# Kernel tuning notes

Hardware: AMD Instinct MI355X
Metric: run time of the kernel (lower is better)

The kernel has to match this reference:

```python
import jax, jax.numpy as jnp
import numpy as np

B, S, N, C = 64, 512, 207, 1
H = 256
D = N * C          # flattened node-feature size (input_size * n_nodes)
DIN = 2 * D        # GRU input size with concat_mask=True


def setup_inputs() -> dict:
    key = jax.random.key(0)
    ks = jax.random.split(key, 8)
    x = jax.random.normal(ks[0], (B, S, N, C), dtype=jnp.float32)
    mask = (jax.random.uniform(ks[1], (B, S, N, C)) < 0.8).astype(jnp.float32)
    bnd = 1.0 / np.sqrt(H)  # torch default init bound for GRUCell and Linear(H, D)
    u = lambda k, shp: jax.random.uniform(k, shp, minval=-bnd, maxval=bnd, dtype=jnp.float32)
    return {
        'x': x,
        'mask': mask,
        'W_ih': u(ks[2], (3 * H, DIN)),
        'W_hh': u(ks[3], (3 * H, H)),
        'b_ih': u(ks[4], (3 * H,)),
        'b_hh': u(ks[5], (3 * H,)),
        'W_ro': u(ks[6], (D, H)),
        'b_ro': u(ks[7], (D,)),
    }


def _gru_cell(x_t, h, W_ih, W_hh, b_ih, b_hh):
    gi = x_t @ W_ih.T + b_ih              # [B, 3H]
    gh = h @ W_hh.T + b_hh                # [B, 3H]
    i_r, i_z, i_n = jnp.split(gi, 3, axis=-1)
    h_r, h_z, h_n = jnp.split(gh, 3, axis=-1)
    r = jax.nn.sigmoid(i_r + h_r)
    z = jax.nn.sigmoid(i_z + h_z)
    n = jnp.tanh(i_n + r * h_n)
    return (1.0 - z) * n + z * h


def reference(x, mask, W_ih, W_hh, b_ih, b_hh, W_ro, b_ro):
    b, s, n_nodes, c = x.shape
    xf = x.reshape(b, s, n_nodes * c)       # 'b s n c -> b s (n c)'
    mf = mask.reshape(b, s, n_nodes * c)
    h0 = jnp.zeros((b, H), dtype=x.dtype)   # state_init='zero'
    xhat0 = h0 @ W_ro.T + b_ro              # readout of initial state

    def step(carry, inp):
        h, x_hat = carry
        x_t, m_t = inp                       # [B, D] each
        x_p = jnp.where(m_t > 0.5, x_t, x_hat)
        x_in = jnp.concatenate([x_p, m_t], axis=-1)  # concat_mask
        h_new = _gru_cell(x_in, h, W_ih, W_hh, b_ih, b_hh)
        x_hat_new = h_new @ W_ro.T + b_ro
        return (h_new, x_hat_new), x_hat_new

    # scan over steps 0..S-2, time axis leading
    xs = (jnp.swapaxes(xf[:, :-1], 0, 1), jnp.swapaxes(mf[:, :-1], 0, 1))
    _, preds = jax.lax.scan(step, (h0, xhat0), xs)           # [S-1, B, D]
    preds = jnp.concatenate([xhat0[None], preds], axis=0)    # [S, B, D]
    x_hat = jnp.swapaxes(preds, 0, 1).reshape(b, s, n_nodes, c)
    return x_hat
```

## Files before the change

kernel.cpp:

```cpp
#include <hip/hip_runtime.h>
#include <math.h>

#define BB 64
#define SS 512
#define DD 207
#define HH 256
#define NWG 64
#define LDW 676
#define ROW 260
#define AG __HIP_MEMORY_SCOPE_AGENT

#define SROWS 672
#define HOFF  416
#define SLOT  (SROWS * 64)
#define BUF_FLOATS ((size_t)SS * SLOT)
#define FLAG_U32 (64 * 32)
#define STAGE_FLOATS ((size_t)SS * DD * 64)
#define WS_NEED6 ((BUF_FLOATS + FLAG_U32 + STAGE_FLOATS) * sizeof(float))

#define V3_AROWS 928
#define V3_HBASE 416
#define V3_ACT (V3_AROWS * 64)
#define V3_FLAGS (64 * 32)
#define V3_WS_SMALL ((size_t)(V3_ACT + V3_FLAGS) * sizeof(float))
#define V3_WS_FULL  ((size_t)(V3_ACT + V3_FLAGS + STAGE_FLOATS) * sizeof(float))

__device__ __forceinline__ void ast4(float* p, float v) {
    union { float f; unsigned u; } c; c.f = v;
    __hip_atomic_store((unsigned*)p, c.u, __ATOMIC_RELAXED, AG);
}

__device__ __forceinline__ void run_range6(
    const float4* __restrict__ A4, const float* __restrict__ wgl,
    float* __restrict__ red, int u, int bp, int wc0, int gr0, int len, int slot)
{
    float4 c0 = make_float4(0.f, 0.f, 0.f, 0.f);
    float4 c1 = c0, c2 = c0;
    #pragma unroll 4
    for (int k = 0; k < len; k += 4) {
        float4 a0 = A4[(gr0 + k + 0) * 16 + bp];
        float4 a1 = A4[(gr0 + k + 1) * 16 + bp];
        float4 a2 = A4[(gr0 + k + 2) * 16 + bp];
        float4 a3 = A4[(gr0 + k + 3) * 16 + bp];
        float4 w0 = *(const float4*)&wgl[(0 + u) * LDW + wc0 + k];
        float4 w1 = *(const float4*)&wgl[(4 + u) * LDW + wc0 + k];
        float4 w2 = *(const float4*)&wgl[(8 + u) * LDW + wc0 + k];
        c0.x += a0.x*w0.x + a1.x*w0.y + a2.x*w0.z + a3.x*w0.w;
        c0.y += a0.y*w0.x + a1.y*w0.y + a2.y*w0.z + a3.y*w0.w;
        c0.z += a0.z*w0.x + a1.z*w0.y + a2.z*w0.z + a3.z*w0.w;
        c0.w += a0.w*w0.x + a1.w*w0.y + a2.w*w0.z + a3.w*w0.w;
        c1.x += a0.x*w1.x + a1.x*w1.y + a2.x*w1.z + a3.x*w1.w;
        c1.y += a0.y*w1.x + a1.y*w1.y + a2.y*w1.z + a3.y*w1.w;
        c1.z += a0.z*w1.x + a1.z*w1.y + a2.z*w1.z + a3.z*w1.w;
        c1.w += a0.w*w1.x + a1.w*w1.y + a2.w*w1.z + a3.w*w1.w;
        c2.x += a0.x*w2.x + a1.x*w2.y + a2.x*w2.z + a3.x*w2.w;
        c2.y += a0.y*w2.x + a1.y*w2.y + a2.y*w2.z + a3.y*w2.w;
        c2.z += a0.z*w2.x + a1.z*w2.y + a2.z*w2.z + a3.z*w2.w;
        c2.w += a0.w*w2.x + a1.w*w2.y + a2.w*w2.z + a3.w*w2.w;
    }
    float4* R4 = (float4*)red;
    R4[(slot * 12 + 0 + u) * 16 + bp] = c0;
    R4[(slot * 12 + 4 + u) * 16 + bp] = c1;
    R4[(slot * 12 + 8 + u) * 16 + bp] = c2;
}

__global__ __launch_bounds__(256) void rnn_init6(float* __restrict__ ws) {
    int i = blockIdx.x * blockDim.x + threadIdx.x;
    for (int idx = i; idx < HH * 64; idx += gridDim.x * blockDim.x)
        ws[HOFF * 64 + idx] = 0.f;
    unsigned* fl = (unsigned*)(ws + BUF_FLOATS);
    for (int idx = i; idx < FLAG_U32; idx += gridDim.x * blockDim.x)
        fl[idx] = 0u;
}

__global__ __launch_bounds__(256) void rnn_persist6(
    const float* __restrict__ x, const float* __restrict__ mask,
    const float* __restrict__ W_ih, const float* __restrict__ W_hh,
    const float* __restrict__ b_ih, const float* __restrict__ b_hh,
    const float* __restrict__ W_ro, const float* __restrict__ b_ro,
    float* __restrict__ ws, float* __restrict__ out)
{
    const int wg = blockIdx.x;
    const int tid = threadIdx.x;
    const int lane = tid & 63;
    const int wv = tid >> 6;

    float* buf = ws;
    unsigned* flags = (unsigned*)(ws + BUF_FLOATS);
    float* stage = ws + BUF_FLOATS + FLAG_U32;

    __shared__ float wgl[12 * LDW];
    __shared__ float wrol[4 * ROW];
    __shared__ float red[8 * 12 * 64];
    __shared__ float redB[16 * 64];
    __shared__ float hloc[4 * 64];
    __shared__ float bihl[12], bhhl[12], brol[4];

    const int d0 = (207 * wg) / NWG;
    const int d1 = (207 * (wg + 1)) / NWG;
    const int dc = d1 - d0;

    for (int i = tid; i < 12 * LDW; i += 256) {
        int r = i / LDW, c = i - r * LDW;
        int rg = (r >> 2) * 256 + wg * 4 + (r & 3);
        float v = 0.f;
        if (c < 414) v = W_ih[rg * 414 + c];
        else if (c >= 416 && c < 672) v = W_hh[rg * 256 + (c - 416)];
        wgl[i] = v;
    }
    for (int i = tid; i < 4 * 256; i += 256) {
        int dl_ = i >> 8, j = i & 255;
        wrol[dl_ * ROW + j] = (dl_ < dc) ? W_ro[(d0 + dl_) * 256 + j] : 0.f;
    }
    if (tid < 12) {
        int rg = (tid >> 2) * 256 + wg * 4 + (tid & 3);
        bihl[tid] = b_ih[rg];
        bhhl[tid] = b_hh[rg];
    }
    if (tid < 4) brol[tid] = (tid < dc) ? b_ro[d0 + tid] : 0.f;
    hloc[tid] = 0.f;
    __syncthreads();

    const float4* A4 = (const float4*)buf;
    const int u  = lane >> 4;
    const int bp = lane & 15;

    const bool have = (tid < dc * 64);
    const int dl = tid >> 6, b = tid & 63;
    const size_t gbase = (size_t)b * (SS * DD) + (d0 + dl);
    float xv_pf = 0.f, mv_pf = 0.f;
    if (have) { xv_pf = x[gbase]; mv_pf = mask[gbase]; }

    unsigned gen = 0;

    for (int t = 0; t < SS; ++t) {
        const int sbase = t * SROWS;

        {
            const float* hrow = buf + (size_t)(sbase + HOFF) * 64;
            const int jb = wv * 64;
            float acc0 = 0.f, acc1 = 0.f, acc2 = 0.f, acc3 = 0.f;
            #pragma unroll 4
            for (int j = 0; j < 64; j += 4) {
                float a0 = hrow[(jb + j + 0) * 64 + lane];
                float a1 = hrow[(jb + j + 1) * 64 + lane];
                float a2 = hrow[(jb + j + 2) * 64 + lane];
                float a3 = hrow[(jb + j + 3) * 64 + lane];
                float4 w0 = *(const float4*)&wrol[0 * ROW + jb + j];
                float4 w1 = *(const float4*)&wrol[1 * ROW + jb + j];
                float4 w2 = *(const float4*)&wrol[2 * ROW + jb + j];
                float4 w3 = *(const float4*)&wrol[3 * ROW + jb + j];
                acc0 += a0*w0.x + a1*w0.y + a2*w0.z + a3*w0.w;
                acc1 += a0*w1.x + a1*w1.y + a2*w1.z + a3*w1.w;
                acc2 += a0*w2.x + a1*w2.y + a2*w2.z + a3*w2.w;
                acc3 += a0*w3.x + a1*w3.y + a2*w3.z + a3*w3.w;
            }
            redB[(wv * 4 + 0) * 64 + lane] = acc0;
            redB[(wv * 4 + 1) * 64 + lane] = acc1;
            redB[(wv * 4 + 2) * 64 + lane] = acc2;
            redB[(wv * 4 + 3) * 64 + lane] = acc3;
        }
        __syncthreads();
        if (have) {
            float xh = redB[(0 * 4 + dl) * 64 + b] + redB[(1 * 4 + dl) * 64 + b]
                     + redB[(2 * 4 + dl) * 64 + b] + redB[(3 * 4 + dl) * 64 + b]
                     + brol[dl];
            stage[(t * DD + d0 + dl) * 64 + b] = xh;
            if (t < SS - 1) {
                float xi = (mv_pf > 0.5f) ? xv_pf : xh;
                ast4(&buf[(size_t)(sbase + d0 + dl) * 64 + b], xi);
                ast4(&buf[(size_t)(sbase + 207 + d0 + dl) * 64 + b], mv_pf);
            }
        }
        if (t == SS - 1) break;

        ++gen;
        asm volatile("s_waitcnt vmcnt(0)" ::: "memory");
        __syncthreads();
        if (tid == 0)
            __hip_atomic_store(&flags[wg * 32], gen, __ATOMIC_RELAXED, AG);

        run_range6(A4, wgl, red, u, bp, 416 + wv * 64, sbase + HOFF + wv * 64, 64, 4 + wv);

        if (tid < 64) {
            unsigned* f = &flags[tid * 32];
            while (__hip_atomic_load(f, __ATOMIC_RELAXED, AG) < gen) {}
        }
        __syncthreads();

        run_range6(A4, wgl, red, u, bp, wv * 104, sbase + wv * 104, 104, wv);
        __syncthreads();

        {
            const int u2 = tid >> 6, b2 = tid & 63;
            float gir = bihl[0 + u2], giz = bihl[4 + u2], gin = bihl[8 + u2];
            float ghr = bhhl[0 + u2], ghz = bhhl[4 + u2], ghn = bhhl[8 + u2];
            #pragma unroll
            for (int s = 0; s < 4; ++s) {
                gir += red[(s * 12 + 0 + u2) * 64 + b2];
                giz += red[(s * 12 + 4 + u2) * 64 + b2];
                gin += red[(s * 12 + 8 + u2) * 64 + b2];
                ghr += red[((4 + s) * 12 + 0 + u2) * 64 + b2];
                ghz += red[((4 + s) * 12 + 4 + u2) * 64 + b2];
                ghn += red[((4 + s) * 12 + 8 + u2) * 64 + b2];
            }
            float r = 1.f / (1.f + __expf(-(gir + ghr)));
            float z = 1.f / (1.f + __expf(-(giz + ghz)));
            float n = tanhf(gin + r * ghn);
            float hn = (1.f - z) * n + z * hloc[u2 * 64 + b2];
            hloc[u2 * 64 + b2] = hn;
            ast4(&buf[(size_t)((t + 1) * SROWS + HOFF + wg * 4 + u2) * 64 + b2], hn);
        }

        ++gen;
        asm volatile("s_waitcnt vmcnt(0)" ::: "memory");
        __syncthreads();
        if (tid == 0)
            __hip_atomic_store(&flags[wg * 32], gen, __ATOMIC_RELAXED, AG);

        if (have && t + 1 < SS - 1) {
            xv_pf = x[gbase + (size_t)(t + 1) * DD];
            mv_pf = mask[gbase + (size_t)(t + 1) * DD];
        }

        if (tid < 64) {
            unsigned* f = &flags[tid * 32];
            while (__hip_atomic_load(f, __ATOMIC_RELAXED, AG) < gen) {}
        }
        __syncthreads();
    }
}

__global__ __launch_bounds__(256) void out_transpose(
    const float* __restrict__ stage, float* __restrict__ out)
{
    __shared__ float lds[DD * 65];
    const int t = blockIdx.x;
    const float* st = stage + (size_t)t * DD * 64;
    for (int i = threadIdx.x; i < DD * 64; i += 256) {
        int d = i >> 6, b = i & 63;
        lds[d * 65 + b] = st[i];
    }
    __syncthreads();
    for (int i = threadIdx.x; i < DD * 64; i += 256) {
        int b = i / DD, d = i - b * DD;
        out[(size_t)b * (SS * DD) + (size_t)t * DD + d] = lds[d * 65 + b];
    }
}

__device__ __forceinline__ void v3_gbar(unsigned* flags, int wg, unsigned g) {
    __syncthreads();
    if (threadIdx.x < 64) {
        if (threadIdx.x == 0) {
            __builtin_amdgcn_fence(__ATOMIC_RELEASE, "agent");
            __hip_atomic_store(&flags[wg * 32], g, __ATOMIC_RELAXED, AG);
        }
        unsigned* f = &flags[threadIdx.x * 32];
        while (__hip_atomic_load(f, __ATOMIC_RELAXED, AG) < g) { }
        __builtin_amdgcn_fence(__ATOMIC_ACQUIRE, "agent");
    }
    __syncthreads();
}

__global__ __launch_bounds__(256) void v3_init(float* __restrict__ ws) {
    int i = blockIdx.x * blockDim.x + threadIdx.x;
    const int nz = (672 - 414) * 64;
    for (int idx = i; idx < nz; idx += gridDim.x * blockDim.x)
        ws[414 * 64 + idx] = 0.f;
    for (int idx = i; idx < V3_FLAGS; idx += gridDim.x * blockDim.x)
        ((unsigned*)(ws + V3_ACT))[idx] = 0u;
}

template<bool STAGE>
__global__ __launch_bounds__(256) void v3_persist(
    const float* __restrict__ x, const float* __restrict__ mask,
    const float* __restrict__ W_ih, const float* __restrict__ W_hh,
    const float* __restrict__ b_ih, const float* __restrict__ b_hh,
    const float* __restrict__ W_ro, const float* __restrict__ b_ro,
    float* __restrict__ ws, float* __restrict__ out)
{
    const int wg = blockIdx.x;
    const int tid = threadIdx.x;
    const int lane = tid & 63;
    const int wv = tid >> 6;

    float* actg = ws;
    unsigned* flags = (unsigned*)(ws + V3_ACT);
    float* stage = ws + V3_ACT + V3_FLAGS;

    __shared__ float wgl[12 * LDW];
    __shared__ float wrol[4 * 256];
    __shared__ float red[5 * 12 * 64];
    __shared__ float redB[16 * 64];
    __shared__ float hloc[4 * 64];
    __shared__ float bihl[12], bhhl[12], brol[4];

    const int d0 = (207 * wg) / NWG;
    const int d1 = (207 * (wg + 1)) / NWG;
    const int dc = d1 - d0;

    for (int i = tid; i < 12 * LDW; i += 256) {
        int r = i / LDW, c = i - r * LDW;
        int rg = (r >> 2) * 256 + wg * 4 + (r & 3);
        float v = 0.f;
        if (c < 414) v = W_ih[rg * 414 + c];
        else if (c >= 416 && c < 672) v = W_hh[rg * 256 + (c - 416)];
        wgl[i] = v;
    }
    for (int i = tid; i < 4 * 256; i += 256) {
        int dl_ = i >> 8, j = i & 255;
        wrol[i] = (dl_ < dc) ? W_ro[(d0 + dl_) * 256 + j] : 0.f;
    }
    if (tid < 12) {
        int rg = (tid >> 2) * 256 + wg * 4 + (tid & 3);
        bihl[tid] = b_ih[rg];
        bhhl[tid] = b_hh[rg];
    }
    if (tid < 4) brol[tid] = (tid < dc) ? b_ro[d0 + tid] : 0.f;
    hloc[tid] = 0.f;
    __syncthreads();

    const float4* A4 = (const float4*)actg;
    const int u = lane >> 4;
    const int bp = lane & 15;

    const bool have = (tid < dc * 64);
    const int dl = tid >> 6, b = tid & 63;
    const size_t gbase = (size_t)b * (SS * DD) + (d0 + dl);
    float xv_pf = 0.f, mv_pf = 0.f;
    if (have) { xv_pf = x[gbase]; mv_pf = mask[gbase]; }

    unsigned gen = 0;

    for (int t = 0; t < SS; ++t) {
        const int par = t & 1;
        const int hrow0 = V3_HBASE + par * 256;

        {
            const float* hrow = actg + hrow0 * 64;
            const int jb = wv * 64;
            float acc0 = 0.f, acc1 = 0.f, acc2 = 0.f, acc3 = 0.f;
            #pragma unroll 4
            for (int j = 0; j < 64; j += 4) {
                float a0 = hrow[(jb + j + 0) * 64 + lane];
                float a1 = hrow[(jb + j + 1) * 64 + lane];
                float a2 = hrow[(jb + j + 2) * 64 + lane];
                float a3 = hrow[(jb + j + 3) * 64 + lane];
                float4 w0 = *(const float4*)&wrol[0 * 256 + jb + j];
                float4 w1 = *(const float4*)&wrol[1 * 256 + jb + j];
                float4 w2 = *(const float4*)&wrol[2 * 256 + jb + j];
                float4 w3 = *(const float4*)&wrol[3 * 256 + jb + j];
                acc0 += a0*w0.x + a1*w0.y + a2*w0.z + a3*w0.w;
                acc1 += a0*w1.x + a1*w1.y + a2*w1.z + a3*w1.w;
                acc2 += a0*w2.x + a1*w2.y + a2*w2.z + a3*w2.w;
                acc3 += a0*w3.x + a1*w3.y + a2*w3.z + a3*w3.w;
            }
            redB[(wv * 4 + 0) * 64 + lane] = acc0;
            redB[(wv * 4 + 1) * 64 + lane] = acc1;
            redB[(wv * 4 + 2) * 64 + lane] = acc2;
            redB[(wv * 4 + 3) * 64 + lane] = acc3;
        }
        __syncthreads();
        if (have) {
            float xh = redB[(0 * 4 + dl) * 64 + b] + redB[(1 * 4 + dl) * 64 + b]
                     + redB[(2 * 4 + dl) * 64 + b] + redB[(3 * 4 + dl) * 64 + b]
                     + brol[dl];
            if (STAGE) stage[(t * DD + d0 + dl) * 64 + b] = xh;
            else       out[gbase + (size_t)t * DD] = xh;
            if (t < SS - 1) {
                float xi = (mv_pf > 0.5f) ? xv_pf : xh;
                actg[(d0 + dl) * 64 + b] = xi;
                actg[(207 + d0 + dl) * 64 + b] = mv_pf;
            }
        }
        if (t == SS - 1) break;

        if (have && t + 1 < SS - 1) {
            xv_pf = x[gbase + (size_t)(t + 1) * DD];
            mv_pf = mask[gbase + (size_t)(t + 1) * DD];
        }

        v3_gbar(flags, wg, ++gen);

        if (wv == 0)      run_range6(A4, wgl, red, u, bp, 0,   0,          168, 0);
        else if (wv == 1) run_range6(A4, wgl, red, u, bp, 168, 168,        168, 1);
        else if (wv == 2) {
            run_range6(A4, wgl, red, u, bp, 336, 336,        80,  2);
            run_range6(A4, wgl, red, u, bp, 416, hrow0,      96,  3);
        } else            run_range6(A4, wgl, red, u, bp, 512, hrow0 + 96, 160, 4);
        __syncthreads();
        {
            const int u2 = tid >> 6, b2 = tid & 63;
            float gir = red[(0*12 + 0 + u2)*64 + b2] + red[(1*12 + 0 + u2)*64 + b2]
                      + red[(2*12 + 0 + u2)*64 + b2] + bihl[0 + u2];
            float giz = red[(0*12 + 4 + u2)*64 + b2] + red[(1*12 + 4 + u2)*64 + b2]
                      + red[(2*12 + 4 + u2)*64 + b2] + bihl[4 + u2];
            float gin = red[(0*12 + 8 + u2)*64 + b2] + red[(1*12 + 8 + u2)*64 + b2]
                      + red[(2*12 + 8 + u2)*64 + b2] + bihl[8 + u2];
            float ghr = red[(3*12 + 0 + u2)*64 + b2] + red[(4*12 + 0 + u2)*64 + b2] + bhhl[0 + u2];
            float ghz = red[(3*12 + 4 + u2)*64 + b2] + red[(4*12 + 4 + u2)*64 + b2] + bhhl[4 + u2];
            float ghn = red[(3*12 + 8 + u2)*64 + b2] + red[(4*12 + 8 + u2)*64 + b2] + bhhl[8 + u2];
            float r = 1.f / (1.f + __expf(-(gir + ghr)));
            float z = 1.f / (1.f + __expf(-(giz + ghz)));
            float n = tanhf(gin + r * ghn);
            float hn = (1.f - z) * n + z * hloc[u2 * 64 + b2];
            hloc[u2 * 64 + b2] = hn;
            actg[(V3_HBASE + (par ^ 1) * 256 + wg * 4 + u2) * 64 + b2] = hn;
        }
        v3_gbar(flags, wg, ++gen);
    }
}

__global__ __launch_bounds__(768) void rnn_fallback(
    const float* __restrict__ x, const float* __restrict__ mask,
    const float* __restrict__ W_ih, const float* __restrict__ W_hh,
    const float* __restrict__ b_ih, const float* __restrict__ b_hh,
    const float* __restrict__ W_ro, const float* __restrict__ b_ro,
    float* __restrict__ out)
{
    const int b = blockIdx.x, tid = threadIdx.x;
    __shared__ float h[HH];
    __shared__ float hnew[HH];
    __shared__ float xin[414 + 2];
    __shared__ float gi[768];
    __shared__ float gh[768];
    __shared__ float xhat[DD];
    const float bih = b_ih[tid], bhh = b_hh[tid];
    const float bro = (tid < DD) ? b_ro[tid] : 0.f;
    if (tid < HH) h[tid] = 0.f;
    if (tid < DD) xhat[tid] = bro;
    __syncthreads();
    const float* xb = x + (size_t)b * SS * DD;
    const float* mb = mask + (size_t)b * SS * DD;
    float* ob = out + (size_t)b * SS * DD;
    for (int t = 0; t < SS; ++t) {
        if (tid < DD) ob[t * DD + tid] = xhat[tid];
        if (t == SS - 1) break;
        if (tid < DD) {
            float m = mb[t * DD + tid], xv = xb[t * DD + tid];
            xin[tid] = (m > 0.5f) ? xv : xhat[tid];
            xin[DD + tid] = m;
        }
        __syncthreads();
        float accI = bih, accH = bhh;
        const float* wi = W_ih + (size_t)tid * 414;
        for (int k = 0; k < 414; ++k) accI += wi[k] * xin[k];
        const float* wh = W_hh + (size_t)tid * HH;
        for (int k = 0; k < HH; ++k) accH += wh[k] * h[k];
        gi[tid] = accI; gh[tid] = accH;
        __syncthreads();
        if (tid < HH) {
            float r = 1.f / (1.f + __expf(-(gi[tid] + gh[tid])));
            float z = 1.f / (1.f + __expf(-(gi[HH + tid] + gh[HH + tid])));
            float n = tanhf(gi[2 * HH + tid] + r * gh[2 * HH + tid]);
            hnew[tid] = (1.f - z) * n + z * h[tid];
        }
        __syncthreads();
        if (tid < DD) {
            float acc = bro;
            const float* wr = W_ro + (size_t)tid * HH;
            for (int k = 0; k < HH; ++k) acc += wr[k] * hnew[k];
            xhat[tid] = acc;
        }
        if (tid < HH) h[tid] = hnew[tid];
        __syncthreads();
    }
}

extern "C" void kernel_launch(void* const* d_in, const int* in_sizes, int n_in,
                              void* d_out, int out_size, void* d_ws, size_t ws_size,
                              hipStream_t stream) {
    const float* x    = (const float*)d_in[0];
    const float* mask = (const float*)d_in[1];
    const float* W_ih = (const float*)d_in[2];
    const float* W_hh = (const float*)d_in[3];
    const float* b_ih = (const float*)d_in[4];
    const float* b_hh = (const float*)d_in[5];
    const float* W_ro = (const float*)d_in[6];
    const float* b_ro = (const float*)d_in[7];
    float* out = (float*)d_out;
    float* ws  = (float*)d_ws;

    if (ws_size >= WS_NEED6) {
        hipLaunchKernelGGL(rnn_init6, dim3(64), dim3(256), 0, stream, ws);
        hipLaunchKernelGGL(rnn_persist6, dim3(NWG), dim3(256), 0, stream,
                           x, mask, W_ih, W_hh, b_ih, b_hh, W_ro, b_ro, ws, out);
        hipLaunchKernelGGL(out_transpose, dim3(SS), dim3(256), 0, stream,
                           ws + BUF_FLOATS + FLAG_U32, out);
    } else if (ws_size >= V3_WS_FULL) {
        hipLaunchKernelGGL(v3_init, dim3(32), dim3(256), 0, stream, ws);
        hipLaunchKernelGGL((v3_persist<true>), dim3(NWG), dim3(256), 0, stream,
                           x, mask, W_ih, W_hh, b_ih, b_hh, W_ro, b_ro, ws, out);
        hipLaunchKernelGGL(out_transpose, dim3(SS), dim3(256), 0, stream,
                           ws + V3_ACT + V3_FLAGS, out);
    } else if (ws_size >= V3_WS_SMALL) {
        hipLaunchKernelGGL(v3_init, dim3(32), dim3(256), 0, stream, ws);
        hipLaunchKernelGGL((v3_persist<false>), dim3(NWG), dim3(256), 0, stream,
                           x, mask, W_ih, W_hh, b_ih, b_hh, W_ro, b_ro, ws, out);
    } else {
        hipLaunchKernelGGL(rnn_fallback, dim3(BB), dim3(768), 0, stream,
                           x, mask, W_ih, W_hh, b_ih, b_hh, W_ro, b_ro, out);
    }
}
```

Baseline: 6.140 ms.

## Pin persistent GRU workgroups to a single XCD with 512-thread blocks

Launches 256 workgroups, reads each one's XCC id from a hardware register, and keeps only 32 blocks that land on the same XCD. Each surviving 512-thread block owns 8 hidden units instead of 4, which halves the number of participants in the per-step global barrier. When a probe confirms that all ranks share one XCD and see each other's writes, activation and hidden-state stores become plain stores instead of agent-scope atomics. The goal is to shorten the cross-workgroup barrier and make shared state cheaper to exchange through a single XCD's L2, at the cost of a more complex election handshake. It also leaves most of the device idle and depends on at least 32 blocks being scheduled on one XCD.

```diff
diff --git a/kernel.cpp b/kernel.cpp
--- a/kernel.cpp
+++ b/kernel.cpp
@@ -5,7 +5,6 @@
 #define SS 512
 #define DD 207
 #define HH 256
-#define NWG 64
 #define LDW 676
 #define ROW 260
 #define AG __HIP_MEMORY_SCOPE_AGENT
@@ -16,7 +15,14 @@
 #define BUF_FLOATS ((size_t)SS * SLOT)
 #define FLAG_U32 (64 * 32)
 #define STAGE_FLOATS ((size_t)SS * DD * 64)
-#define WS_NEED6 ((BUF_FLOATS + FLAG_U32 + STAGE_FLOATS) * sizeof(float))
+#define WS_NEED7 ((BUF_FLOATS + FLAG_U32 + STAGE_FLOATS) * sizeof(float))
+#define NW 32
+#define BS7 512
+#define GRID7 256
+#define HWREG_XCC (20 | (31 << 11))
+#define MAGICF 1.0e30f
+
+#define R0 ((size_t)(SS - 1) * SLOT)
 
 #define V3_AROWS 928
 #define V3_HBASE 416
@@ -24,10 +30,323 @@
 #define V3_FLAGS (64 * 32)
 #define V3_WS_SMALL ((size_t)(V3_ACT + V3_FLAGS) * sizeof(float))
 #define V3_WS_FULL  ((size_t)(V3_ACT + V3_FLAGS + STAGE_FLOATS) * sizeof(float))
+#define NWG 64
 
 __device__ __forceinline__ void ast4(float* p, float v) {
     union { float f; unsigned u; } c; c.f = v;
     __hip_atomic_store((unsigned*)p, c.u, __ATOMIC_RELAXED, AG);
+}
+
+__global__ __launch_bounds__(256) void rnn_init7(float* __restrict__ ws) {
+    int i = blockIdx.x * blockDim.x + threadIdx.x;
+    for (int idx = i; idx < HH * 64; idx += gridDim.x * blockDim.x)
+        ws[HOFF * 64 + idx] = 0.f;
+    unsigned* fl = (unsigned*)(ws + BUF_FLOATS);
+    for (int idx = i; idx < FLAG_U32; idx += gridDim.x * blockDim.x)
+        fl[idx] = 0u;
+    unsigned* rc = (unsigned*)(ws + R0);
+    for (int idx = i; idx < 2048; idx += gridDim.x * blockDim.x)
+        rc[idx] = 0u;
+    if (i == 0) ((int*)rc)[257] = -1;
+}
+
+__global__ __launch_bounds__(BS7) void rnn_persist7(
+    const float* __restrict__ x, const float* __restrict__ mask,
+    const float* __restrict__ W_ih, const float* __restrict__ W_hh,
+    const float* __restrict__ b_ih, const float* __restrict__ b_hh,
+    const float* __restrict__ W_ro, const float* __restrict__ b_ro,
+    float* __restrict__ ws, float* __restrict__ out)
+{
+    const int tid = threadIdx.x;
+    float* buf = ws;
+    unsigned* flags = (unsigned*)(ws + BUF_FLOATS);
+    float* stage = ws + BUF_FLOATS + FLAG_U32;
+    unsigned* rc   = (unsigned*)(ws + R0);
+    unsigned* rpro = rc + 512;
+    float*    rmag = ws + R0 + 2048;
+
+    __shared__ int sh_rank, sh_xcc, sh_fast;
+
+    if (tid == 0) {
+        unsigned xcc = (unsigned)__builtin_amdgcn_s_getreg(HWREG_XCC);
+        unsigned xb = xcc & 7;
+        unsigned rank = __hip_atomic_fetch_add(&rc[xb * 32], 1u, __ATOMIC_RELAXED, AG);
+        unsigned tot  = __hip_atomic_fetch_add(&rc[256], 1u, __ATOMIC_RELAXED, AG);
+        int* chosen = (int*)&rc[257];
+        if (rank == NW - 1) {
+            int exp = -1;
+            __hip_atomic_compare_exchange_strong(chosen, &exp, (int)xb,
+                __ATOMIC_RELAXED, __ATOMIC_RELAXED, AG);
+        }
+        if (tot == GRID7 - 1) {
+            unsigned best = 0; int bi = 0;
+            for (int q = 0; q < 8; ++q) {
+                unsigned c = __hip_atomic_load(&rc[q * 32], __ATOMIC_RELAXED, AG);
+                if (c > best) { best = c; bi = q; }
+            }
+            int exp = -1;
+            __hip_atomic_compare_exchange_strong(chosen, &exp, bi,
+                __ATOMIC_RELAXED, __ATOMIC_RELAXED, AG);
+        }
+        int c;
+        do { c = __hip_atomic_load(chosen, __ATOMIC_RELAXED, AG); } while (c == -1);
+        sh_rank = (c == (int)xb && rank < NW) ? (int)rank : -1;
+        sh_xcc = (int)xcc;
+        sh_fast = 0;
+    }
+    __syncthreads();
+    const int rank = sh_rank;
+    if (rank < 0) return;
+    const int myxcc = sh_xcc;
+
+    unsigned gen = 0;
+
+    if (tid == 0) {
+        rmag[rank * 32] = MAGICF;
+        __hip_atomic_store(&rpro[rank * 32], (unsigned)myxcc, __ATOMIC_RELAXED, AG);
+    }
+    ++gen;
+    asm volatile("s_waitcnt vmcnt(0)" ::: "memory");
+    __syncthreads();
+    if (tid == 0) __hip_atomic_store(&flags[rank * 32], gen, __ATOMIC_RELAXED, AG);
+    if (tid < NW) {
+        unsigned* f = &flags[tid * 32];
+        while (__hip_atomic_load(f, __ATOMIC_RELAXED, AG) < gen) {}
+    }
+    __syncthreads();
+    if (tid < NW) {
+        float mg = rmag[tid * 32];
+        unsigned pb = __hip_atomic_load(&rpro[tid * 32], __ATOMIC_RELAXED, AG);
+        if (mg != MAGICF || pb != (unsigned)myxcc)
+            __hip_atomic_fetch_or(&rc[258], 1u, __ATOMIC_RELAXED, AG);
+    }
+    ++gen;
+    asm volatile("s_waitcnt vmcnt(0)" ::: "memory");
+    __syncthreads();
+    if (tid == 0) __hip_atomic_store(&flags[rank * 32], gen, __ATOMIC_RELAXED, AG);
+    if (tid < NW) {
+        unsigned* f = &flags[tid * 32];
+        while (__hip_atomic_load(f, __ATOMIC_RELAXED, AG) < gen) {}
+    }
+    __syncthreads();
+    if (tid == 0)
+        sh_fast = (__hip_atomic_load(&rc[258], __ATOMIC_RELAXED, AG) == 0) ? 1 : 0;
+    __syncthreads();
+    const bool fast = (sh_fast != 0);
+
+    __shared__ float wgl[24 * LDW];
+    __shared__ float wrol[8 * ROW];
+    __shared__ float red[8 * 24 * 64];
+    __shared__ float red2[8 * 8 * 64];
+    __shared__ float redB[8 * 8 * 64];
+    __shared__ float hloc[8 * 64];
+    __shared__ float bihl[24], bhhl[24], brol[8];
+
+    const int d0 = (207 * rank) / NW;
+    const int d1 = (207 * (rank + 1)) / NW;
+    const int dc = d1 - d0;
+
+    for (int i = tid; i < 24 * LDW; i += BS7) {
+        int r = i / LDW, c = i - r * LDW;
+        int rg = (r >> 3) * 256 + rank * 8 + (r & 7);
+        float v = 0.f;
+        if (c < 414) v = W_ih[rg * 414 + c];
+        else if (c >= 416 && c < 672) v = W_hh[rg * 256 + (c - 416)];
+        wgl[i] = v;
+    }
+    for (int i = tid; i < 8 * 256; i += BS7) {
+        int dl_ = i >> 8, j = i & 255;
+        wrol[dl_ * ROW + j] = (dl_ < dc) ? W_ro[(d0 + dl_) * 256 + j] : 0.f;
+    }
+    if (tid < 24) {
+        int rg = (tid >> 3) * 256 + rank * 8 + (tid & 7);
+        bihl[tid] = b_ih[rg];
+        bhhl[tid] = b_hh[rg];
+    }
+    if (tid < 8) brol[tid] = (tid < dc) ? b_ro[d0 + tid] : 0.f;
+    hloc[tid] = 0.f;
+    __syncthreads();
+
+    const float4* A4 = (const float4*)buf;
+    const int lane = tid & 63;
+    const int wv = tid >> 6;
+    const int u  = lane >> 4;
+    const int bp = lane & 15;
+
+    const bool have = (tid < dc * 64);
+    const int dl = tid >> 6, b = tid & 63;
+    const size_t gbase = (size_t)b * (SS * DD) + (d0 + dl);
+    float xv_pf = 0.f, mv_pf = 0.f;
+    if (have) { xv_pf = x[gbase]; mv_pf = mask[gbase]; }
+
+    for (int t = 0; t < SS; ++t) {
+        const int sbase = t * SROWS;
+
+        {
+            float4 r0 = make_float4(0.f,0.f,0.f,0.f), r1 = r0;
+            const int kb = wv * 32;
+            #pragma unroll 2
+            for (int k = 0; k < 32; k += 4) {
+                float4 a0 = A4[(sbase + HOFF + kb + k + 0) * 16 + bp];
+                float4 a1 = A4[(sbase + HOFF + kb + k + 1) * 16 + bp];
+                float4 a2 = A4[(sbase + HOFF + kb + k + 2) * 16 + bp];
+                float4 a3 = A4[(sbase + HOFF + kb + k + 3) * 16 + bp];
+                float4 w0 = *(const float4*)&wrol[u * ROW + kb + k];
+                float4 w1 = *(const float4*)&wrol[(u + 4) * ROW + kb + k];
+                r0.x += a0.x*w0.x + a1.x*w0.y + a2.x*w0.z + a3.x*w0.w;
+                r0.y += a0.y*w0.x + a1.y*w0.y + a2.y*w0.z + a3.y*w0.w;
+                r0.z += a0.z*w0.x + a1.z*w0.y + a2.z*w0.z + a3.z*w0.w;
+                r0.w += a0.w*w0.x + a1.w*w0.y + a2.w*w0.z + a3.w*w0.w;
+                r1.x += a0.x*w1.x + a1.x*w1.y + a2.x*w1.z + a3.x*w1.w;
+                r1.y += a0.y*w1.x + a1.y*w1.y + a2.y*w1.z + a3.y*w1.w;
+                r1.z += a0.z*w1.x + a1.z*w1.y + a2.z*w1.z + a3.z*w1.w;
+                r1.w += a0.w*w1.x + a1.w*w1.y + a2.w*w1.z + a3.w*w1.w;
+            }
+            float4* RB = (float4*)redB;
+            RB[(wv * 8 + u) * 16 + bp] = r0;
+            RB[(wv * 8 + u + 4) * 16 + bp] = r1;
+        }
+        __syncthreads();
+        if (have) {
+            float xh = brol[dl];
+            #pragma unroll
+            for (int w8 = 0; w8 < 8; ++w8) xh += redB[(w8 * 8 + dl) * 64 + b];
+            stage[((size_t)t * DD + d0 + dl) * 64 + b] = xh;
+            if (t < SS - 1) {
+                float xi = (mv_pf > 0.5f) ? xv_pf : xh;
+                float* p0 = &buf[(size_t)(sbase + d0 + dl) * 64 + b];
+                float* p1 = &buf[(size_t)(sbase + 207 + d0 + dl) * 64 + b];
+                if (fast) { *p0 = xi; *p1 = mv_pf; }
+                else      { ast4(p0, xi); ast4(p1, mv_pf); }
+            }
+        }
+        if (t == SS - 1) break;
+
+        ++gen;
+        asm volatile("s_waitcnt vmcnt(0)" ::: "memory");
+        __syncthreads();
+        if (tid == 0) __hip_atomic_store(&flags[rank * 32], gen, __ATOMIC_RELAXED, AG);
+
+        float4 acc[6];
+        #pragma unroll
+        for (int j = 0; j < 6; ++j) acc[j] = make_float4(0.f,0.f,0.f,0.f);
+        float4 accN0 = make_float4(0.f,0.f,0.f,0.f), accN1 = accN0;
+        {
+            const int wc0 = 416 + wv * 32, gr0 = sbase + HOFF + wv * 32;
+            #pragma unroll 2
+            for (int k = 0; k < 32; k += 4) {
+                float4 a0 = A4[(gr0 + k + 0) * 16 + bp];
+                float4 a1 = A4[(gr0 + k + 1) * 16 + bp];
+                float4 a2 = A4[(gr0 + k + 2) * 16 + bp];
+                float4 a3 = A4[(gr0 + k + 3) * 16 + bp];
+                #pragma unroll
+                for (int j = 0; j < 4; ++j) {
+                    float4 w = *(const float4*)&wgl[(u + 4 * j) * LDW + wc0 + k];
+                    acc[j].x += a0.x*w.x + a1.x*w.y + a2.x*w.z + a3.x*w.w;
+                    acc[j].y += a0.y*w.x + a1.y*w.y + a2.y*w.z + a3.y*w.w;
+                    acc[j].z += a0.z*w.x + a1.z*w.y + a2.z*w.z + a3.z*w.w;
+                    acc[j].w += a0.w*w.x + a1.w*w.y + a2.w*w.z + a3.w*w.w;
+                }
+                float4 wn0 = *(const float4*)&wgl[(16 + u) * LDW + wc0 + k];
+                float4 wn1 = *(const float4*)&wgl[(20 + u) * LDW + wc0 + k];
+                accN0.x += a0.x*wn0.x + a1.x*wn0.y + a2.x*wn0.z + a3.x*wn0.w;
+                accN0.y += a0.y*wn0.x + a1.y*wn0.y + a2.y*wn0.z + a3.y*wn0.w;
+                accN0.z += a0.z*wn0.x + a1.z*wn0.y + a2.z*wn0.z + a3.z*wn0.w;
+                accN0.w += a0.w*wn0.x + a1.w*wn0.y + a2.w*wn0.z + a3.w*wn0.w;
+                accN1.x += a0.x*wn1.x + a1.x*wn1.y + a2.x*wn1.z + a3.x*wn1.w;
+                accN1.y += a0.y*wn1.x + a1.y*wn1.y + a2.y*wn1.z + a3.y*wn1.w;
+                accN1.z += a0.z*wn1.x + a1.z*wn1.y + a2.z*wn1.z + a3.z*wn1.w;
+                accN1.w += a0.w*wn1.x + a1.w*wn1.y + a2.w*wn1.z + a3.w*wn1.w;
+            }
+        }
+        {
+            float4* R2 = (float4*)red2;
+            R2[(wv * 8 + u) * 16 + bp] = accN0;
+            R2[(wv * 8 + u + 4) * 16 + bp] = accN1;
+        }
+
+        if (tid < NW) {
+            unsigned* f = &flags[tid * 32];
+            while (__hip_atomic_load(f, __ATOMIC_RELAXED, AG) < gen) {}
+        }
+        __syncthreads();
+
+        {
+            const int wc0 = wv * 52, gr0 = sbase + wv * 52;
+            #pragma unroll 2
+            for (int k = 0; k < 52; k += 4) {
+                float4 a0 = A4[(gr0 + k + 0) * 16 + bp];
+                float4 a1 = A4[(gr0 + k + 1) * 16 + bp];
+                float4 a2 = A4[(gr0 + k + 2) * 16 + bp];
+                float4 a3 = A4[(gr0 + k + 3) * 16 + bp];
+                #pragma unroll
+                for (int j = 0; j < 6; ++j) {
+                    float4 w = *(const float4*)&wgl[(u + 4 * j) * LDW + wc0 + k];
+                    acc[j].x += a0.x*w.x + a1.x*w.y + a2.x*w.z + a3.x*w.w;
+                    acc[j].y += a0.y*w.x + a1.y*w.y + a2.y*w.z + a3.y*w.w;
+                    acc[j].z += a0.z*w.x + a1.z*w.y + a2.z*w.z + a3.z*w.w;
+                    acc[j].w += a0.w*w.x + a1.w*w.y + a2.w*w.z + a3.w*w.w;
+                }
+            }
+            float4* R4 = (float4*)red;
+            #pragma unroll
+            for (int j = 0; j < 6; ++j)
+                R4[(wv * 24 + u + 4 * j) * 16 + bp] = acc[j];
+        }
+        __syncthreads();
+
+        {
+            const int uu = tid >> 6, b2 = tid & 63;
+            float sr = 0.f, sz = 0.f, sni = 0.f, snh = 0.f;
+            #pragma unroll
+            for (int w8 = 0; w8 < 8; ++w8) {
+                sr  += red[(w8 * 24 + 0 + uu) * 64 + b2];
+                sz  += red[(w8 * 24 + 8 + uu) * 64 + b2];
+                sni += red[(w8 * 24 + 16 + uu) * 64 + b2];
+                snh += red2[(w8 * 8 + uu) * 64 + b2];
+            }
+            float r = 1.f / (1.f + __expf(-(sr + bihl[0 + uu] + bhhl[0 + uu])));
+            float z = 1.f / (1.f + __expf(-(sz + bihl[8 + uu] + bhhl[8 + uu])));
+            float n = tanhf(sni + bihl[16 + uu] + r * (snh + bhhl[16 + uu]));
+            float hn = (1.f - z) * n + z * hloc[tid];
+            hloc[tid] = hn;
+            float* hp = &buf[(size_t)((t + 1) * SROWS + HOFF + rank * 8 + uu) * 64 + b2];
+            if (fast) *hp = hn; else ast4(hp, hn);
+        }
+
+        ++gen;
+        asm volatile("s_waitcnt vmcnt(0)" ::: "memory");
+        __syncthreads();
+        if (tid == 0) __hip_atomic_store(&flags[rank * 32], gen, __ATOMIC_RELAXED, AG);
+
+        if (have && t + 1 < SS - 1) {
+            xv_pf = x[gbase + (size_t)(t + 1) * DD];
+            mv_pf = mask[gbase + (size_t)(t + 1) * DD];
+        }
+
+        if (tid < NW) {
+            unsigned* f = &flags[tid * 32];
+            while (__hip_atomic_load(f, __ATOMIC_RELAXED, AG) < gen) {}
+        }
+        __syncthreads();
+    }
+}
+
+__global__ __launch_bounds__(256) void out_transpose(
+    const float* __restrict__ stage, float* __restrict__ out)
+{
+    __shared__ float lds[DD * 65];
+    const int t = blockIdx.x;
+    const float* st = stage + (size_t)t * DD * 64;
+    for (int i = threadIdx.x; i < DD * 64; i += 256) {
+        int d = i >> 6, b = i & 63;
+        lds[d * 65 + b] = st[i];
+    }
+    __syncthreads();
+    for (int i = threadIdx.x; i < DD * 64; i += 256) {
+        int b = i / DD, d = i - b * DD;
+        out[(size_t)b * (SS * DD) + (size_t)t * DD + d] = lds[d * 65 + b];
+    }
 }
 
 __device__ __forceinline__ void run_range6(
@@ -64,190 +383,6 @@
     R4[(slot * 12 + 8 + u) * 16 + bp] = c2;
 }
 
-__global__ __launch_bounds__(256) void rnn_init6(float* __restrict__ ws) {
-    int i = blockIdx.x * blockDim.x + threadIdx.x;
-    for (int idx = i; idx < HH * 64; idx += gridDim.x * blockDim.x)
-        ws[HOFF * 64 + idx] = 0.f;
-    unsigned* fl = (unsigned*)(ws + BUF_FLOATS);
-    for (int idx = i; idx < FLAG_U32; idx += gridDim.x * blockDim.x)
-        fl[idx] = 0u;
-}
-
-__global__ __launch_bounds__(256) void rnn_persist6(
-    const float* __restrict__ x, const float* __restrict__ mask,
-    const float* __restrict__ W_ih, const float* __restrict__ W_hh,
-    const float* __restrict__ b_ih, const float* __restrict__ b_hh,
-    const float* __restrict__ W_ro, const float* __restrict__ b_ro,
-    float* __restrict__ ws, float* __restrict__ out)
-{
-    const int wg = blockIdx.x;
-    const int tid = threadIdx.x;
-    const int lane = tid & 63;
-    const int wv = tid >> 6;
-
-    float* buf = ws;
-    unsigned* flags = (unsigned*)(ws + BUF_FLOATS);
-    float* stage = ws + BUF_FLOATS + FLAG_U32;
-
-    __shared__ float wgl[12 * LDW];
-    __shared__ float wrol[4 * ROW];
-    __shared__ float red[8 * 12 * 64];
-    __shared__ float redB[16 * 64];
-    __shared__ float hloc[4 * 64];
-    __shared__ float bihl[12], bhhl[12], brol[4];
-
-    const int d0 = (207 * wg) / NWG;
-    const int d1 = (207 * (wg + 1)) / NWG;
-    const int dc = d1 - d0;
-
-    for (int i = tid; i < 12 * LDW; i += 256) {
-        int r = i / LDW, c = i - r * LDW;
-        int rg = (r >> 2) * 256 + wg * 4 + (r & 3);
-        float v = 0.f;
-        if (c < 414) v = W_ih[rg * 414 + c];
-        else if (c >= 416 && c < 672) v = W_hh[rg * 256 + (c - 416)];
-        wgl[i] = v;
-    }
-    for (int i = tid; i < 4 * 256; i += 256) {
-        int dl_ = i >> 8, j = i & 255;
-        wrol[dl_ * ROW + j] = (dl_ < dc) ? W_ro[(d0 + dl_) * 256 + j] : 0.f;
-    }
-    if (tid < 12) {
-        int rg = (tid >> 2) * 256 + wg * 4 + (tid & 3);
-        bihl[tid] = b_ih[rg];
-        bhhl[tid] = b_hh[rg];
-    }
-    if (tid < 4) brol[tid] = (tid < dc) ? b_ro[d0 + tid] : 0.f;
-    hloc[tid] = 0.f;
-    __syncthreads();
-
-    const float4* A4 = (const float4*)buf;
-    const int u  = lane >> 4;
-    const int bp = lane & 15;
-
-    const bool have = (tid < dc * 64);
-    const int dl = tid >> 6, b = tid & 63;
-    const size_t gbase = (size_t)b * (SS * DD) + (d0 + dl);
-    float xv_pf = 0.f, mv_pf = 0.f;
-    if (have) { xv_pf = x[gbase]; mv_pf = mask[gbase]; }
-
-    unsigned gen = 0;
-
-    for (int t = 0; t < SS; ++t) {
-        const int sbase = t * SROWS;
-
-        {
-            const float* hrow = buf + (size_t)(sbase + HOFF) * 64;
-            const int jb = wv * 64;
-            float acc0 = 0.f, acc1 = 0.f, acc2 = 0.f, acc3 = 0.f;
-            #pragma unroll 4
-            for (int j = 0; j < 64; j += 4) {
-                float a0 = hrow[(jb + j + 0) * 64 + lane];
-                float a1 = hrow[(jb + j + 1) * 64 + lane];
-                float a2 = hrow[(jb + j + 2) * 64 + lane];
-                float a3 = hrow[(jb + j + 3) * 64 + lane];
-                float4 w0 = *(const float4*)&wrol[0 * ROW + jb + j];
-                float4 w1 = *(const float4*)&wrol[1 * ROW + jb + j];
-                float4 w2 = *(const float4*)&wrol[2 * ROW + jb + j];
-                float4 w3 = *(const float4*)&wrol[3 * ROW + jb + j];
-                acc0 += a0*w0.x + a1*w0.y + a2*w0.z + a3*w0.w;
-                acc1 += a0*w1.x + a1*w1.y + a2*w1.z + a3*w1.w;
-                acc2 += a0*w2.x + a1*w2.y + a2*w2.z + a3*w2.w;
-                acc3 += a0*w3.x + a1*w3.y + a2*w3.z + a3*w3.w;
-            }
-            redB[(wv * 4 + 0) * 64 + lane] = acc0;
-            redB[(wv * 4 + 1) * 64 + lane] = acc1;
-            redB[(wv * 4 + 2) * 64 + lane] = acc2;
-            redB[(wv * 4 + 3) * 64 + lane] = acc3;
-        }
-        __syncthreads();
-        if (have) {
-            float xh = redB[(0 * 4 + dl) * 64 + b] + redB[(1 * 4 + dl) * 64 + b]
-                     + redB[(2 * 4 + dl) * 64 + b] + redB[(3 * 4 + dl) * 64 + b]
-                     + brol[dl];
-            stage[(t * DD + d0 + dl) * 64 + b] = xh;
-            if (t < SS - 1) {
-                float xi = (mv_pf > 0.5f) ? xv_pf : xh;
-                ast4(&buf[(size_t)(sbase + d0 + dl) * 64 + b], xi);
-                ast4(&buf[(size_t)(sbase + 207 + d0 + dl) * 64 + b], mv_pf);
-            }
-        }
-        if (t == SS - 1) break;
-
-        ++gen;
-        asm volatile("s_waitcnt vmcnt(0)" ::: "memory");
-        __syncthreads();
-        if (tid == 0)
-            __hip_atomic_store(&flags[wg * 32], gen, __ATOMIC_RELAXED, AG);
-
-        run_range6(A4, wgl, red, u, bp, 416 + wv * 64, sbase + HOFF + wv * 64, 64, 4 + wv);
-
-        if (tid < 64) {
-            unsigned* f = &flags[tid * 32];
-            while (__hip_atomic_load(f, __ATOMIC_RELAXED, AG) < gen) {}
-        }
-        __syncthreads();
-
-        run_range6(A4, wgl, red, u, bp, wv * 104, sbase + wv * 104, 104, wv);
-        __syncthreads();
-
-        {
-            const int u2 = tid >> 6, b2 = tid & 63;
-            float gir = bihl[0 + u2], giz = bihl[4 + u2], gin = bihl[8 + u2];
-            float ghr = bhhl[0 + u2], ghz = bhhl[4 + u2], ghn = bhhl[8 + u2];
-            #pragma unroll
-            for (int s = 0; s < 4; ++s) {
-                gir += red[(s * 12 + 0 + u2) * 64 + b2];
-                giz += red[(s * 12 + 4 + u2) * 64 + b2];
-                gin += red[(s * 12 + 8 + u2) * 64 + b2];
-                ghr += red[((4 + s) * 12 + 0 + u2) * 64 + b2];
-                ghz += red[((4 + s) * 12 + 4 + u2) * 64 + b2];
-                ghn += red[((4 + s) * 12 + 8 + u2) * 64 + b2];
-            }
-            float r = 1.f / (1.f + __expf(-(gir + ghr)));
-            float z = 1.f / (1.f + __expf(-(giz + ghz)));
-            float n = tanhf(gin + r * ghn);
-            float hn = (1.f - z) * n + z * hloc[u2 * 64 + b2];
-            hloc[u2 * 64 + b2] = hn;
-            ast4(&buf[(size_t)((t + 1) * SROWS + HOFF + wg * 4 + u2) * 64 + b2], hn);
-        }
-
-        ++gen;
-        asm volatile("s_waitcnt vmcnt(0)" ::: "memory");
-        __syncthreads();
-        if (tid == 0)
-            __hip_atomic_store(&flags[wg * 32], gen, __ATOMIC_RELAXED, AG);
-
-        if (have && t + 1 < SS - 1) {
-            xv_pf = x[gbase + (size_t)(t + 1) * DD];
-            mv_pf = mask[gbase + (size_t)(t + 1) * DD];
-        }
-
-        if (tid < 64) {
-            unsigned* f = &flags[tid * 32];
-            while (__hip_atomic_load(f, __ATOMIC_RELAXED, AG) < gen) {}
-        }
-        __syncthreads();
-    }
-}
-
-__global__ __launch_bounds__(256) void out_transpose(
-    const float* __restrict__ stage, float* __restrict__ out)
-{
-    __shared__ float lds[DD * 65];
-    const int t = blockIdx.x;
-    const float* st = stage + (size_t)t * DD * 64;
-    for (int i = threadIdx.x; i < DD * 64; i += 256) {
-        int d = i >> 6, b = i & 63;
-        lds[d * 65 + b] = st[i];
-    }
-    __syncthreads();
-    for (int i = threadIdx.x; i < DD * 64; i += 256) {
-        int b = i / DD, d = i - b * DD;
-        out[(size_t)b * (SS * DD) + (size_t)t * DD + d] = lds[d * 65 + b];
-    }
-}
-
 __device__ __forceinline__ void v3_gbar(unsigned* flags, int wg, unsigned g) {
     __syncthreads();
     if (threadIdx.x < 64) {
@@ -283,22 +418,18 @@
     const int tid = threadIdx.x;
     const int lane = tid & 63;
     const int wv = tid >> 6;
-
     float* actg = ws;
     unsigned* flags = (unsigned*)(ws + V3_ACT);
     float* stage = ws + V3_ACT + V3_FLAGS;
-
     __shared__ float wgl[12 * LDW];
     __shared__ float wrol[4 * 256];
     __shared__ float red[5 * 12 * 64];
     __shared__ float redB[16 * 64];
     __shared__ float hloc[4 * 64];
     __shared__ float bihl[12], bhhl[12], brol[4];
-
     const int d0 = (207 * wg) / NWG;
     const int d1 = (207 * (wg + 1)) / NWG;
     const int dc = d1 - d0;
-
     for (int i = tid; i < 12 * LDW; i += 256) {
         int r = i / LDW, c = i - r * LDW;
         int rg = (r >> 2) * 256 + wg * 4 + (r & 3);
@@ -319,23 +450,18 @@
     if (tid < 4) brol[tid] = (tid < dc) ? b_ro[d0 + tid] : 0.f;
     hloc[tid] = 0.f;
     __syncthreads();
-
     const float4* A4 = (const float4*)actg;
     const int u = lane >> 4;
     const int bp = lane & 15;
-
     const bool have = (tid < dc * 64);
     const int dl = tid >> 6, b = tid & 63;
     const size_t gbase = (size_t)b * (SS * DD) + (d0 + dl);
     float xv_pf = 0.f, mv_pf = 0.f;
     if (have) { xv_pf = x[gbase]; mv_pf = mask[gbase]; }
-
     unsigned gen = 0;
-
     for (int t = 0; t < SS; ++t) {
         const int par = t & 1;
         const int hrow0 = V3_HBASE + par * 256;
-
         {
             const float* hrow = actg + hrow0 * 64;
             const int jb = wv * 64;
@@ -374,14 +500,11 @@
             }
         }
         if (t == SS - 1) break;
-
         if (have && t + 1 < SS - 1) {
             xv_pf = x[gbase + (size_t)(t + 1) * DD];
             mv_pf = mask[gbase + (size_t)(t + 1) * DD];
         }
-
         v3_gbar(flags, wg, ++gen);
-
         if (wv == 0)      run_range6(A4, wgl, red, u, bp, 0,   0,          168, 0);
         else if (wv == 1) run_range6(A4, wgl, red, u, bp, 168, 168,        168, 1);
         else if (wv == 2) {
@@ -481,9 +604,9 @@
     float* out = (float*)d_out;
     float* ws  = (float*)d_ws;
 
-    if (ws_size >= WS_NEED6) {
-        hipLaunchKernelGGL(rnn_init6, dim3(64), dim3(256), 0, stream, ws);
-        hipLaunchKernelGGL(rnn_persist6, dim3(NWG), dim3(256), 0, stream,
+    if (ws_size >= WS_NEED7) {
+        hipLaunchKernelGGL(rnn_init7, dim3(64), dim3(256), 0, stream, ws);
+        hipLaunchKernelGGL(rnn_persist7, dim3(GRID7), dim3(BS7), 0, stream,
                            x, mask, W_ih, W_hh, b_ih, b_hh, W_ro, b_ro, ws, out);
         hipLaunchKernelGGL(out_transpose, dim3(SS), dim3(256), 0, stream,
                            ws + BUF_FLOATS + FLAG_U32, out);
```

Result: slower. 7.089 ms (+15.4%).
